# Kernel optimization log

Measured on AMD Instinct MI355X. Metric: run time of the kernel, lower is better.

Reference implementation:

```python
import jax, jax.numpy as jnp
import numpy as np

N = 500_000
D = 128           # input_dim
A = 128           # attention_dim
O = 1             # output_dim (broadcasts over input_dim)
B = 256           # number of repertoires (segments)


def setup_inputs() -> dict:
    key = jax.random.key(0)
    k1, k2, k3, k4 = jax.random.split(key, 4)
    x = jax.random.normal(k1, (N, D), dtype=jnp.float32)
    batch_index = jnp.sort(jax.random.randint(k2, (N,), 0, B, dtype=jnp.int32))
    # attention MLP params: Linear(D->A), Tanh, Linear(A->O)
    W1 = jax.random.normal(k3, (D, A), dtype=jnp.float32) * (1.0 / np.sqrt(D))
    b1 = jnp.zeros((A,), dtype=jnp.float32)
    W2 = jax.random.normal(k4, (A, O), dtype=jnp.float32) * (1.0 / np.sqrt(A))
    b2 = jnp.zeros((O,), dtype=jnp.float32)
    return {"x": x, "batch_index": batch_index, "W1": W1, "b1": b1, "W2": W2, "b2": b2}


def reference(x, batch_index, W1, b1, W2, b2):
    # per-instance attention score: Linear -> Tanh -> Linear
    h = jnp.tanh(x @ W1 + b1)          # [N, A]
    scores = h @ W2 + b2               # [N, O]
    # segment softmax over instances within each repertoire
    seg_max = jax.ops.segment_max(scores, batch_index, num_segments=B)   # [B, O]
    e = jnp.exp(scores - seg_max[batch_index])                           # [N, O]
    denom = jax.ops.segment_sum(e, batch_index, num_segments=B)          # [B, O]
    w = e / denom[batch_index]                                           # [N, O]
    # weighted sum of instance features per repertoire (O=1 broadcasts over D)
    out = jax.ops.segment_sum(w * x, batch_index, num_segments=B)        # [B, D]
    return out
```

## Files before the change

kernel.cpp:

```cpp
#include <hip/hip_runtime.h>
#include <math.h>

#define D_DIM 128
#define A_DIM 128
#define NTHREADS 512

typedef _Float16 f16x8 __attribute__((ext_vector_type(8)));
typedef __attribute__((ext_vector_type(4))) float f32x4;

__device__ __forceinline__ float fast_tanh(float v) {
    float e = __expf(2.0f * v);
    return 1.0f - 2.0f * __builtin_amdgcn_rcpf(e + 1.0f);
}

__device__ __forceinline__ int lower_bound_i32(const int* __restrict__ arr, int n, int val) {
    int lo = 0, hi = n;
    while (lo < hi) {
        int mid = (lo + hi) >> 1;
        if (arr[mid] < val) lo = mid + 1; else hi = mid;
    }
    return lo;
}

extern "C" __global__ void __launch_bounds__(NTHREADS)
fused_attn_kernel(const float* __restrict__ x,
                  const int* __restrict__ bidx,
                  const float* __restrict__ W1,
                  const float* __restrict__ b1,
                  const float* __restrict__ W2,
                  float* __restrict__ out,
                  int N, int B)
{
    __shared__ _Float16 w1s[A_DIM * D_DIM];
    __shared__ float sB1[A_DIM];
    __shared__ float sW2[A_DIM];
    __shared__ float s_lds[128];
    __shared__ float o_red[8 * 4 * 32];
    __shared__ int   seg_bounds[2];

    const int tid = threadIdx.x;
    const int b   = blockIdx.x;

    if (tid == 0) {
        seg_bounds[0] = lower_bound_i32(bidx, N, b);
        seg_bounds[1] = lower_bound_i32(bidx, N, b + 1);
    }
    if (tid < A_DIM) { sB1[tid] = b1[tid]; sW2[tid] = W2[tid]; }

    for (int item = tid; item < A_DIM * 16; item += NTHREADS) {
        const int c = item & (A_DIM - 1);
        const int chunk = item >> 7;
        f16x8 vh;
        #pragma unroll
        for (int j = 0; j < 8; ++j)
            vh[j] = (_Float16)W1[(chunk * 8 + j) * A_DIM + c];
        const int addr = c * 256 + ((chunk ^ (c & 15)) << 4);
        *reinterpret_cast<f16x8*>(reinterpret_cast<char*>(w1s) + addr) = vh;
    }
    __syncthreads();

    const int lo = seg_bounds[0], hi = seg_bounds[1];
    const int len = hi - lo;

    if (len <= 0) {
        if (tid < D_DIM) out[b * D_DIM + tid] = 0.0f;
        return;
    }

    const int lane = tid & 63;
    const int wv   = tid >> 6;
    const int lc   = lane & 15;
    const int lg   = lane >> 4;
    const int nt   = (len + 127) >> 7;

    float m = -INFINITY;
    float denom = 0.0f;
    float o_part[32];
    #pragma unroll
    for (int v = 0; v < 32; ++v) o_part[v] = 0.0f;

    float4 buf[8];
    {
        const int gi = min(lo + wv * 16 + lc, N - 1);
        const float4* xr = reinterpret_cast<const float4*>(x + (size_t)gi * D_DIM);
        #pragma unroll
        for (int ks = 0; ks < 4; ++ks) {
            buf[2*ks]   = xr[ks*8 + lg*2];
            buf[2*ks+1] = xr[ks*8 + lg*2 + 1];
        }
    }

    for (int tile = 0; tile < nt; ++tile) {
        f16x8 ah[4], al[4];
        #pragma unroll
        for (int ks = 0; ks < 4; ++ks) {
            float vv[8] = {buf[2*ks].x, buf[2*ks].y, buf[2*ks].z, buf[2*ks].w,
                           buf[2*ks+1].x, buf[2*ks+1].y, buf[2*ks+1].z, buf[2*ks+1].w};
            #pragma unroll
            for (int j = 0; j < 8; ++j) {
                float xv = vv[j];
                _Float16 h = (_Float16)xv;
                ah[ks][j] = h;
                al[ks][j] = (_Float16)(xv - (float)h);
            }
        }

        if (tile + 1 < nt) {
            const int gi = min(lo + (tile + 1) * 128 + wv * 16 + lc, N - 1);
            const float4* xr = reinterpret_cast<const float4*>(x + (size_t)gi * D_DIM);
            #pragma unroll
            for (int ks = 0; ks < 4; ++ks) {
                buf[2*ks]   = xr[ks*8 + lg*2];
                buf[2*ks+1] = xr[ks*8 + lg*2 + 1];
            }
        }

        float part0 = 0.f, part1 = 0.f, part2 = 0.f, part3 = 0.f;
        #pragma unroll
        for (int t = 0; t < 8; ++t) {
            f32x4 acc = {0.f, 0.f, 0.f, 0.f};
            const int c = t * 16 + lc;
            const char* base = reinterpret_cast<const char*>(w1s) + c * 256;
            #pragma unroll
            for (int ks = 0; ks < 4; ++ks) {
                const int chunk = ks * 4 + lg;
                f16x8 bh = *reinterpret_cast<const f16x8*>(
                    base + ((chunk ^ (c & 15)) << 4));
                acc = __builtin_amdgcn_mfma_f32_16x16x32_f16(ah[ks], bh, acc, 0, 0, 0);
                acc = __builtin_amdgcn_mfma_f32_16x16x32_f16(al[ks], bh, acc, 0, 0, 0);
            }
            const float b1v = sB1[c], w2v = sW2[c];
            part0 += fast_tanh(acc[0] + b1v) * w2v;
            part1 += fast_tanh(acc[1] + b1v) * w2v;
            part2 += fast_tanh(acc[2] + b1v) * w2v;
            part3 += fast_tanh(acc[3] + b1v) * w2v;
        }
        #pragma unroll
        for (int mk = 8; mk >= 1; mk >>= 1) {
            part0 += __shfl_xor(part0, mk);
            part1 += __shfl_xor(part1, mk);
            part2 += __shfl_xor(part2, mk);
            part3 += __shfl_xor(part3, mk);
        }
        if (lc == 0) {
            const int rb = wv * 16 + lg * 4;
            const int gbase = tile * 128 + rb;
            s_lds[rb + 0] = (gbase + 0 < len) ? part0 : -INFINITY;
            s_lds[rb + 1] = (gbase + 1 < len) ? part1 : -INFINITY;
            s_lds[rb + 2] = (gbase + 2 < len) ? part2 : -INFINITY;
            s_lds[rb + 3] = (gbase + 3 < len) ? part3 : -INFINITY;
        }
        __syncthreads();

        const float a0 = s_lds[lane], a1 = s_lds[64 + lane];
        float pm = fmaxf(a0, a1);
        #pragma unroll
        for (int mk = 32; mk >= 1; mk >>= 1) pm = fmaxf(pm, __shfl_xor(pm, mk));
        const float mn = fmaxf(m, pm);
        const float f  = __expf(m - mn);
        float ds = __expf(a0 - mn) + __expf(a1 - mn);
        #pragma unroll
        for (int mk = 32; mk >= 1; mk >>= 1) ds += __shfl_xor(ds, mk);
        denom = denom * f + ds;
        m = mn;

        const float w = __expf(s_lds[wv * 16 + lc] - mn);
        #pragma unroll
        for (int ks = 0; ks < 4; ++ks) {
            #pragma unroll
            for (int j = 0; j < 8; ++j) {
                const int v = ks * 8 + j;
                o_part[v] = fmaf(o_part[v], f,
                                 w * ((float)ah[ks][j] + (float)al[ks][j]));
            }
        }
        __syncthreads();
    }

    #pragma unroll
    for (int v = 0; v < 32; ++v) {
        #pragma unroll
        for (int mk = 8; mk >= 1; mk >>= 1)
            o_part[v] += __shfl_xor(o_part[v], mk);
    }
    if (lc == 0) {
        #pragma unroll
        for (int v = 0; v < 32; ++v)
            o_red[(wv * 4 + lg) * 32 + v] = o_part[v];
    }
    __syncthreads();
    if (tid < 128) {
        const int lg2 = tid >> 5, v = tid & 31;
        float s = 0.0f;
        #pragma unroll
        for (int w2 = 0; w2 < 8; ++w2) s += o_red[(w2 * 4 + lg2) * 32 + v];
        const int d = (v >> 3) * 32 + lg2 * 8 + (v & 7);
        out[b * D_DIM + d] = s / denom;
    }
}

extern "C" void kernel_launch(void* const* d_in, const int* in_sizes, int n_in,
                              void* d_out, int out_size, void* d_ws, size_t ws_size,
                              hipStream_t stream)
{
    const float* x    = (const float*)d_in[0];
    const int*   bidx = (const int*)d_in[1];
    const float* W1   = (const float*)d_in[2];
    const float* b1   = (const float*)d_in[3];
    const float* W2   = (const float*)d_in[4];

    const int N = in_sizes[1];
    const int B = out_size / D_DIM;

    fused_attn_kernel<<<B, NTHREADS, 0, stream>>>(
        x, bidx, W1, b1, W2, (float*)d_out, N, B);
}
```

Measured before the change: 82.60 us.

## Split each segment across four blocks with flash-style partial softmax combine

Each segment is now handled by four 256-thread blocks, each taking interleaved 64-row tiles, instead of one 512-thread block. Every block writes its partial weighted sum, running max and denominator to workspace, and a third kernel merges them with log-sum-exp rescaling. Segment bounds move into a separate binary-search kernel. The aim is more blocks in flight to fill the GPU's compute units, since 256 blocks underfill the device. The cost is two extra kernel launches, a workspace round trip, and reloading W1 into shared memory in four times as many blocks.

```diff
diff --git a/kernel.cpp b/kernel.cpp
--- a/kernel.cpp
+++ b/kernel.cpp
@@ -3,7 +3,10 @@
 
 #define D_DIM 128
 #define A_DIM 128
-#define NTHREADS 512
+#define SPLIT 4
+#define NTHREADS 256
+#define TROWS 64
+#define PSTRIDE 132
 
 typedef _Float16 f16x8 __attribute__((ext_vector_type(8)));
 typedef __attribute__((ext_vector_type(4))) float f32x4;
@@ -22,29 +25,33 @@
     return lo;
 }
 
+extern "C" __global__ void __launch_bounds__(256)
+seg_bounds_kernel(const int* __restrict__ bidx, int N, int B,
+                  int* __restrict__ seg_start)
+{
+    const int i = blockIdx.x * 256 + threadIdx.x;
+    if (i <= B) seg_start[i] = lower_bound_i32(bidx, N, i);
+}
+
 extern "C" __global__ void __launch_bounds__(NTHREADS)
-fused_attn_kernel(const float* __restrict__ x,
-                  const int* __restrict__ bidx,
-                  const float* __restrict__ W1,
-                  const float* __restrict__ b1,
-                  const float* __restrict__ W2,
-                  float* __restrict__ out,
-                  int N, int B)
+fused_partial_kernel(const float* __restrict__ x,
+                     const int* __restrict__ seg_start,
+                     const float* __restrict__ W1,
+                     const float* __restrict__ b1,
+                     const float* __restrict__ W2,
+                     float* __restrict__ part,
+                     int N)
 {
     __shared__ _Float16 w1s[A_DIM * D_DIM];
     __shared__ float sB1[A_DIM];
     __shared__ float sW2[A_DIM];
-    __shared__ float s_lds[128];
-    __shared__ float o_red[8 * 4 * 32];
-    __shared__ int   seg_bounds[2];
+    __shared__ float s_lds[TROWS];
+    __shared__ float o_red[16 * 32];
 
     const int tid = threadIdx.x;
-    const int b   = blockIdx.x;
-
-    if (tid == 0) {
-        seg_bounds[0] = lower_bound_i32(bidx, N, b);
-        seg_bounds[1] = lower_bound_i32(bidx, N, b + 1);
-    }
+    const int b   = blockIdx.x >> 2;
+    const int q   = blockIdx.x & (SPLIT - 1);
+
     if (tid < A_DIM) { sB1[tid] = b1[tid]; sW2[tid] = W2[tid]; }
 
     for (int item = tid; item < A_DIM * 16; item += NTHREADS) {
@@ -59,19 +66,14 @@
     }
     __syncthreads();
 
-    const int lo = seg_bounds[0], hi = seg_bounds[1];
-    const int len = hi - lo;
-
-    if (len <= 0) {
-        if (tid < D_DIM) out[b * D_DIM + tid] = 0.0f;
-        return;
-    }
+    const int lo  = seg_start[b];
+    const int len = seg_start[b + 1] - lo;
+    const int nt  = (len + TROWS - 1) >> 6;
 
     const int lane = tid & 63;
     const int wv   = tid >> 6;
     const int lc   = lane & 15;
     const int lg   = lane >> 4;
-    const int nt   = (len + 127) >> 7;
 
     float m = -INFINITY;
     float denom = 0.0f;
@@ -80,8 +82,8 @@
     for (int v = 0; v < 32; ++v) o_part[v] = 0.0f;
 
     float4 buf[8];
-    {
-        const int gi = min(lo + wv * 16 + lc, N - 1);
+    if (q < nt) {
+        const int gi = min(lo + q * TROWS + wv * 16 + lc, N - 1);
         const float4* xr = reinterpret_cast<const float4*>(x + (size_t)gi * D_DIM);
         #pragma unroll
         for (int ks = 0; ks < 4; ++ks) {
@@ -90,7 +92,7 @@
         }
     }
 
-    for (int tile = 0; tile < nt; ++tile) {
+    for (int tile = q; tile < nt; tile += SPLIT) {
         f16x8 ah[4], al[4];
         #pragma unroll
         for (int ks = 0; ks < 4; ++ks) {
@@ -105,8 +107,9 @@
             }
         }
 
-        if (tile + 1 < nt) {
-            const int gi = min(lo + (tile + 1) * 128 + wv * 16 + lc, N - 1);
+        const int next = tile + SPLIT;
+        if (next < nt) {
+            const int gi = min(lo + next * TROWS + wv * 16 + lc, N - 1);
             const float4* xr = reinterpret_cast<const float4*>(x + (size_t)gi * D_DIM);
             #pragma unroll
             for (int ks = 0; ks < 4; ++ks) {
@@ -144,21 +147,21 @@
         }
         if (lc == 0) {
             const int rb = wv * 16 + lg * 4;
-            const int gbase = tile * 128 + rb;
-            s_lds[rb + 0] = (gbase + 0 < len) ? part0 : -INFINITY;
-            s_lds[rb + 1] = (gbase + 1 < len) ? part1 : -INFINITY;
-            s_lds[rb + 2] = (gbase + 2 < len) ? part2 : -INFINITY;
-            s_lds[rb + 3] = (gbase + 3 < len) ? part3 : -INFINITY;
+            const int grow = tile * TROWS + rb;
+            s_lds[rb + 0] = (grow + 0 < len) ? part0 : -INFINITY;
+            s_lds[rb + 1] = (grow + 1 < len) ? part1 : -INFINITY;
+            s_lds[rb + 2] = (grow + 2 < len) ? part2 : -INFINITY;
+            s_lds[rb + 3] = (grow + 3 < len) ? part3 : -INFINITY;
         }
         __syncthreads();
 
-        const float a0 = s_lds[lane], a1 = s_lds[64 + lane];
-        float pm = fmaxf(a0, a1);
+        const float a0 = s_lds[lane];
+        float pm = a0;
         #pragma unroll
         for (int mk = 32; mk >= 1; mk >>= 1) pm = fmaxf(pm, __shfl_xor(pm, mk));
         const float mn = fmaxf(m, pm);
         const float f  = __expf(m - mn);
-        float ds = __expf(a0 - mn) + __expf(a1 - mn);
+        float ds = __expf(a0 - mn);
         #pragma unroll
         for (int mk = 32; mk >= 1; mk >>= 1) ds += __shfl_xor(ds, mk);
         denom = denom * f + ds;
@@ -189,14 +192,44 @@
             o_red[(wv * 4 + lg) * 32 + v] = o_part[v];
     }
     __syncthreads();
+
+    float* pb = part + (size_t)blockIdx.x * PSTRIDE;
     if (tid < 128) {
         const int lg2 = tid >> 5, v = tid & 31;
         float s = 0.0f;
         #pragma unroll
-        for (int w2 = 0; w2 < 8; ++w2) s += o_red[(w2 * 4 + lg2) * 32 + v];
+        for (int w2 = 0; w2 < 4; ++w2) s += o_red[(w2 * 4 + lg2) * 32 + v];
         const int d = (v >> 3) * 32 + lg2 * 8 + (v & 7);
-        out[b * D_DIM + d] = s / denom;
-    }
+        pb[d] = s;
+    }
+    if (tid == 0) { pb[128] = m; pb[129] = denom; }
+}
+
+extern "C" __global__ void __launch_bounds__(128)
+combine_kernel(const float* __restrict__ part, float* __restrict__ out)
+{
+    const int b = blockIdx.x, d = threadIdx.x;
+    const float* pb = part + (size_t)b * SPLIT * PSTRIDE;
+
+    float mq[SPLIT];
+    float mstar = -INFINITY;
+    #pragma unroll
+    for (int q = 0; q < SPLIT; ++q) {
+        mq[q] = pb[q * PSTRIDE + 128];
+        mstar = fmaxf(mstar, mq[q]);
+    }
+    if (mstar == -INFINITY) {
+        out[b * D_DIM + d] = 0.0f;
+        return;
+    }
+    float den = 0.0f, val = 0.0f;
+    #pragma unroll
+    for (int q = 0; q < SPLIT; ++q) {
+        const float e = __expf(mq[q] - mstar);
+        den = fmaf(pb[q * PSTRIDE + 129], e, den);
+        val = fmaf(pb[q * PSTRIDE + d],   e, val);
+    }
+    out[b * D_DIM + d] = val / den;
 }
 
 extern "C" void kernel_launch(void* const* d_in, const int* in_sizes, int n_in,
@@ -212,6 +245,12 @@
     const int N = in_sizes[1];
     const int B = out_size / D_DIM;
 
-    fused_attn_kernel<<<B, NTHREADS, 0, stream>>>(
-        x, bidx, W1, b1, W2, (float*)d_out, N, B);
-}
+    char* ws = (char*)d_ws;
+    int*   seg_start = (int*)ws;
+    float* part      = (float*)(ws + 4096);
+
+    seg_bounds_kernel<<<(B + 256) / 256, 256, 0, stream>>>(bidx, N, B, seg_start);
+    fused_partial_kernel<<<B * SPLIT, NTHREADS, 0, stream>>>(
+        x, seg_start, W1, b1, W2, part, N);
+    combine_kernel<<<B, 128, 0, stream>>>(part, (float*)d_out);
+}
```

Measured after the change: 88.42 us. 1.07x slower.

## Drop online max softmax and per-tile barriers; waves process independent row tiles

Applied to the files above, without the earlier changes.

Each wave now walks its own 16-row tiles with a stride of eight waves, instead of all waves sharing 128-row block tiles. The online-softmax running max and the block-wide max/sum reductions, with their two barriers per tile, are gone. Scores are exponentiated directly, with per-wave numerators and denominators combined once at the end. This relies on scores being bounded (tanh output times W2) so that exp without a max shift does not overflow, which trades numerical robustness for removing the synchronization.

```diff
diff --git a/kernel.cpp b/kernel.cpp
--- a/kernel.cpp
+++ b/kernel.cpp
@@ -4,6 +4,7 @@
 #define D_DIM 128
 #define A_DIM 128
 #define NTHREADS 512
+#define WPS 8
 
 typedef _Float16 f16x8 __attribute__((ext_vector_type(8)));
 typedef __attribute__((ext_vector_type(4))) float f32x4;
@@ -34,8 +35,8 @@
     __shared__ _Float16 w1s[A_DIM * D_DIM];
     __shared__ float sB1[A_DIM];
     __shared__ float sW2[A_DIM];
-    __shared__ float s_lds[128];
     __shared__ float o_red[8 * 4 * 32];
+    __shared__ float s_d[8];
     __shared__ int   seg_bounds[2];
 
     const int tid = threadIdx.x;
@@ -59,8 +60,8 @@
     }
     __syncthreads();
 
-    const int lo = seg_bounds[0], hi = seg_bounds[1];
-    const int len = hi - lo;
+    const int lo  = seg_bounds[0];
+    const int len = seg_bounds[1] - lo;
 
     if (len <= 0) {
         if (tid < D_DIM) out[b * D_DIM + tid] = 0.0f;
@@ -71,16 +72,15 @@
     const int wv   = tid >> 6;
     const int lc   = lane & 15;
     const int lg   = lane >> 4;
-    const int nt   = (len + 127) >> 7;
-
-    float m = -INFINITY;
-    float denom = 0.0f;
+    const int nt   = (len + 15) >> 4;
+
+    float den = 0.0f;
     float o_part[32];
     #pragma unroll
     for (int v = 0; v < 32; ++v) o_part[v] = 0.0f;
 
     float4 buf[8];
-    {
+    if (wv < nt) {
         const int gi = min(lo + wv * 16 + lc, N - 1);
         const float4* xr = reinterpret_cast<const float4*>(x + (size_t)gi * D_DIM);
         #pragma unroll
@@ -90,23 +90,23 @@
         }
     }
 
-    for (int tile = 0; tile < nt; ++tile) {
+    for (int tile = wv; tile < nt; tile += WPS) {
         f16x8 ah[4], al[4];
         #pragma unroll
         for (int ks = 0; ks < 4; ++ks) {
-            float vv[8] = {buf[2*ks].x, buf[2*ks].y, buf[2*ks].z, buf[2*ks].w,
-                           buf[2*ks+1].x, buf[2*ks+1].y, buf[2*ks+1].z, buf[2*ks+1].w};
             #pragma unroll
             for (int j = 0; j < 8; ++j) {
-                float xv = vv[j];
-                _Float16 h = (_Float16)xv;
+                const float xv = (j < 4) ? ((const float*)&buf[2*ks])[j]
+                                         : ((const float*)&buf[2*ks+1])[j-4];
+                const _Float16 h = (_Float16)xv;
                 ah[ks][j] = h;
                 al[ks][j] = (_Float16)(xv - (float)h);
             }
         }
 
-        if (tile + 1 < nt) {
-            const int gi = min(lo + (tile + 1) * 128 + wv * 16 + lc, N - 1);
+        const int next = tile + WPS;
+        if (next < nt) {
+            const int gi = min(lo + next * 16 + lc, N - 1);
             const float4* xr = reinterpret_cast<const float4*>(x + (size_t)gi * D_DIM);
             #pragma unroll
             for (int ks = 0; ks < 4; ++ks) {
@@ -142,39 +142,25 @@
             part2 += __shfl_xor(part2, mk);
             part3 += __shfl_xor(part3, mk);
         }
-        if (lc == 0) {
-            const int rb = wv * 16 + lg * 4;
-            const int gbase = tile * 128 + rb;
-            s_lds[rb + 0] = (gbase + 0 < len) ? part0 : -INFINITY;
-            s_lds[rb + 1] = (gbase + 1 < len) ? part1 : -INFINITY;
-            s_lds[rb + 2] = (gbase + 2 < len) ? part2 : -INFINITY;
-            s_lds[rb + 3] = (gbase + 3 < len) ? part3 : -INFINITY;
-        }
-        __syncthreads();
-
-        const float a0 = s_lds[lane], a1 = s_lds[64 + lane];
-        float pm = fmaxf(a0, a1);
-        #pragma unroll
-        for (int mk = 32; mk >= 1; mk >>= 1) pm = fmaxf(pm, __shfl_xor(pm, mk));
-        const float mn = fmaxf(m, pm);
-        const float f  = __expf(m - mn);
-        float ds = __expf(a0 - mn) + __expf(a1 - mn);
-        #pragma unroll
-        for (int mk = 32; mk >= 1; mk >>= 1) ds += __shfl_xor(ds, mk);
-        denom = denom * f + ds;
-        m = mn;
-
-        const float w = __expf(s_lds[wv * 16 + lc] - mn);
+        const int src = (lc >> 2) << 4;
+        const float t0 = __shfl(part0, src);
+        const float t1 = __shfl(part1, src);
+        const float t2 = __shfl(part2, src);
+        const float t3 = __shfl(part3, src);
+        const float s01 = (lc & 1) ? t1 : t0;
+        const float s23 = (lc & 1) ? t3 : t2;
+        const float my_s = (lc & 2) ? s23 : s01;
+        const float w = (tile * 16 + lc < len) ? __expf(my_s) : 0.0f;
+        den += w;
+
         #pragma unroll
         for (int ks = 0; ks < 4; ++ks) {
             #pragma unroll
             for (int j = 0; j < 8; ++j) {
                 const int v = ks * 8 + j;
-                o_part[v] = fmaf(o_part[v], f,
-                                 w * ((float)ah[ks][j] + (float)al[ks][j]));
-            }
-        }
-        __syncthreads();
+                o_part[v] = fmaf(w, (float)ah[ks][j] + (float)al[ks][j], o_part[v]);
+            }
+        }
     }
 
     #pragma unroll
@@ -183,19 +169,27 @@
         for (int mk = 8; mk >= 1; mk >>= 1)
             o_part[v] += __shfl_xor(o_part[v], mk);
     }
+    #pragma unroll
+    for (int mk = 8; mk >= 1; mk >>= 1) den += __shfl_xor(den, mk);
+
     if (lc == 0) {
         #pragma unroll
         for (int v = 0; v < 32; ++v)
             o_red[(wv * 4 + lg) * 32 + v] = o_part[v];
+        if (lg == 0) s_d[wv] = den;
     }
     __syncthreads();
+
     if (tid < 128) {
         const int lg2 = tid >> 5, v = tid & 31;
-        float s = 0.0f;
-        #pragma unroll
-        for (int w2 = 0; w2 < 8; ++w2) s += o_red[(w2 * 4 + lg2) * 32 + v];
+        float val = 0.0f;
+        #pragma unroll
+        for (int w2 = 0; w2 < 8; ++w2) val += o_red[(w2 * 4 + lg2) * 32 + v];
+        float dtot = 0.0f;
+        #pragma unroll
+        for (int w2 = 0; w2 < 8; ++w2) dtot += s_d[w2];
         const int d = (v >> 3) * 32 + lg2 * 8 + (v & 7);
-        out[b * D_DIM + d] = s / denom;
+        out[b * D_DIM + d] = val / dtot;
     }
 }
 
```

Result: slower. 130.6 us (+58.2%).
